# Kernel tuning notes

Measured on AMD Instinct MI355X. Metric: run time of the kernel, lower is better.

## Reference

```python
import jax, jax.numpy as jnp
import numpy as np

DECAY = 0.9      # LIF membrane decay per step
V_TH = 1.0       # spike threshold


def setup_inputs() -> dict:
    key = jax.random.key(0)
    k1, k2, k3, k4, k5 = jax.random.split(key, 5)
    B, D, N = 256, 1024, 2048
    density = 0.3
    external_inputs = jax.random.normal(k1, (B, D), dtype=jnp.float32)
    # nn.Linear(input_dim, num_neurons): weight [N, D], bias [N]
    W_in = jax.random.normal(k2, (N, D), dtype=jnp.float32) / np.sqrt(D)
    b_in = jnp.zeros((N,), dtype=jnp.float32)
    adj_weights = jax.random.normal(k3, (N, N), dtype=jnp.float32) * 0.01
    mask = (jax.random.uniform(k4, (N, N)) < density).astype(jnp.float32)
    mask = mask * (1.0 - jnp.eye(N, dtype=jnp.float32))  # zero diagonal
    return {
        "external_inputs": external_inputs,
        "W_in": W_in,
        "b_in": b_in,
        "adj_weights": adj_weights,
        "mask": mask,
        "time_steps": 64,
    }


def _spike(x):
    # Heaviside spike: 1 if membrane exceeds threshold
    return (x >= 0.0).astype(x.dtype)


def reference(external_inputs, W_in, b_in, adj_weights, mask, time_steps):
    B = external_inputs.shape[0]
    N = adj_weights.shape[0]
    I_ext = external_inputs @ W_in.T + b_in              # [B, N]
    W_eff = adj_weights * mask                           # [N, N]
    V0 = jnp.zeros((B, N), dtype=external_inputs.dtype)
    s0 = jnp.zeros((B, N), dtype=external_inputs.dtype)

    def step(carry, _):
        V, s = carry
        I_total = I_ext + s @ W_eff.T                    # recurrent current
        V = DECAY * V + I_total                          # LIF integration
        s_new = _spike(V - V_TH)
        V = V * (1.0 - s_new)                            # reset on spike
        return (V, s_new), s_new

    (_, _), spike_hist = jax.lax.scan(step, (V0, s0), None, length=time_steps)
    return spike_hist.mean(axis=0)                       # [B, N] firing rates
```

## Files before the change

kernel.cpp:

```cpp
#include <hip/hip_runtime.h>
#include <cstdint>
#include <cstddef>

#define N_NEU 2048
#define D_IN  1024
#define T_STEPS 64

typedef _Float16 f16x8 __attribute__((ext_vector_type(8)));
typedef _Float16 f16x4 __attribute__((ext_vector_type(4)));
typedef float    f32x4 __attribute__((ext_vector_type(4)));
typedef unsigned u32x4 __attribute__((ext_vector_type(4)));

#define MFMA16(a, b, c) __builtin_amdgcn_mfma_f32_16x16x32_f16((a), (b), (c), 0, 0, 0)


__device__ inline f16x8 expand8(unsigned b) {
  u32x4 t;
#pragma unroll
  for (int i = 0; i < 4; ++i) {
    unsigned m = (b >> (2 * i)) & 3u;
    unsigned s = (m | (m << 15)) & 0x00010001u;
    t[i] = s * 0x3C00u;
  }
  return __builtin_bit_cast(f16x8, t);
}

__global__ __launch_bounds__(256) void k_wsplit(const float* __restrict__ adj,
                                                const float* __restrict__ mask,
                                                _Float16* __restrict__ Wh,
                                                _Float16* __restrict__ Wl,
                                                unsigned long long* __restrict__ bmv) {
  const int idx = blockIdx.x * 256 + threadIdx.x;
  if (idx < 2 * 256 * 64) bmv[idx] = 0ull;
  const int total4 = (N_NEU * N_NEU) / 4;
  for (int i = idx; i < total4; i += gridDim.x * 256) {
    float4 a = ((const float4*)adj)[i];
    float4 m = ((const float4*)mask)[i];
    float w0 = a.x * m.x, w1 = a.y * m.y, w2 = a.z * m.z, w3 = a.w * m.w;
    f16x4 h, lo;
    h[0] = (_Float16)w0; lo[0] = (_Float16)((w0 - (float)h[0]) * 4096.0f);
    h[1] = (_Float16)w1; lo[1] = (_Float16)((w1 - (float)h[1]) * 4096.0f);
    h[2] = (_Float16)w2; lo[2] = (_Float16)((w2 - (float)h[2]) * 4096.0f);
    h[3] = (_Float16)w3; lo[3] = (_Float16)((w3 - (float)h[3]) * 4096.0f);
    ((f16x4*)Wh)[i] = h;
    ((f16x4*)Wl)[i] = lo;
  }
}

__global__ __launch_bounds__(256) void k_iext(const float* __restrict__ ext,
                                              const float* __restrict__ Win,
                                              const float* __restrict__ bin,
                                              float* __restrict__ Iext) {
  __shared__ float At[32][68];
  __shared__ float Bt[32][68];
  const int tid = threadIdx.x;
  const int b0 = (blockIdx.x & 3) * 64;
  const int n0 = (blockIdx.x >> 2) * 64;
  const int tx = tid & 15, ty = tid >> 4;
  float acc[4][4] = {};
  for (int kt = 0; kt < D_IN / 32; ++kt) {
    const int k0 = kt * 32;
#pragma unroll
    for (int i = 0; i < 8; ++i) {
      int e = tid + i * 256;
      int kk = e & 31, row = e >> 5;
      At[kk][row] = ext[(size_t)(b0 + row) * D_IN + k0 + kk];
      Bt[kk][row] = Win[(size_t)(n0 + row) * D_IN + k0 + kk];
    }
    __syncthreads();
    for (int kk = 0; kk < 32; ++kk) {
      f32x4 a = *(const f32x4*)&At[kk][ty * 4];
      f32x4 b = *(const f32x4*)&Bt[kk][tx * 4];
#pragma unroll
      for (int i = 0; i < 4; ++i)
#pragma unroll
        for (int j = 0; j < 4; ++j) acc[i][j] += a[i] * b[j];
    }
    __syncthreads();
  }
#pragma unroll
  for (int i = 0; i < 4; ++i)
#pragma unroll
    for (int j = 0; j < 4; ++j)
      Iext[(size_t)(b0 + ty * 4 + i) * N_NEU + n0 + tx * 4 + j] = acc[i][j] + bin[n0 + tx * 4 + j];
}

__global__ __launch_bounds__(512, 2) void k_fused11(
    const _Float16* __restrict__ Wh, const _Float16* __restrict__ Wl,
    const float* __restrict__ Iext, unsigned long long* __restrict__ bmv,
    float* __restrict__ out) {
  __shared__ float red[8 * 32 * 32];
  __shared__ unsigned bmA[32 * 64];
  __shared__ unsigned bmB[32 * 64];

  const int tid = threadIdx.x;
  const int lane = tid & 63;
  const int kw = tid >> 6;
  const int l15 = lane & 15;
  const int klo = lane >> 4;
  const int sh = klo * 8;
  const int gp = blockIdx.x >> 6;
  const int ns = blockIdx.x & 63;
  const int n0 = ns * 32;
  const int gA = gp, gB = gp + 4;
  const float inv4096 = 1.0f / 4096.0f;
  const f32x4 z4 = {0.f, 0.f, 0.f, 0.f};

  float IxA[2], IxB[2];
#pragma unroll
  for (int j = 0; j < 2; ++j) {
    IxA[j] = Iext[(size_t)(gA * 32 + j * 16 + (tid >> 5)) * N_NEU + n0 + (tid & 31)];
    IxB[j] = Iext[(size_t)(gB * 32 + j * 16 + (tid >> 5)) * N_NEU + n0 + (tid & 31)];
  }

  const _Float16* whb = Wh + (size_t)(n0 + l15) * N_NEU + kw * 256 + klo * 8;
  const _Float16* wlb = Wl + (size_t)(n0 + l15) * N_NEU + kw * 256 + klo * 8;
  f16x8 whf[2][8], wlf[2][8];
#pragma unroll
  for (int nt = 0; nt < 2; ++nt)
#pragma unroll
    for (int kcl = 0; kcl < 8; ++kcl) {
      whf[nt][kcl] = *(const f16x8*)(whb + nt * 16 * N_NEU + kcl * 32);
      wlf[nt][kcl] = *(const f16x8*)(wlb + nt * 16 * N_NEU + kcl * 32);
    }

  float VA[2] = {0.f, 0.f}, VB[2] = {0.f, 0.f};
  unsigned cA[2] = {0u, 0u}, cB[2] = {0u, 0u};
  unsigned long long vA[4], vB[4];

  auto spec_issue = [&](int g, int buf, unsigned long long (&v)[4]) {
    const unsigned long long* src = bmv + (size_t)buf * 16384 + (size_t)g * 2048 + tid;
#pragma unroll
    for (int i = 0; i < 4; ++i)
      v[i] = __hip_atomic_load(src + (size_t)i * 512, __ATOMIC_RELAXED, __HIP_MEMORY_SCOPE_AGENT);
  };
  auto check_retry = [&](int g, int buf, unsigned want, unsigned long long (&v)[4]) {
    const unsigned long long* src = bmv + (size_t)buf * 16384 + (size_t)g * 2048 + tid;
    unsigned need = 0u;
#pragma unroll
    for (int i = 0; i < 4; ++i)
      if ((unsigned)(v[i] >> 32) != want) need |= 1u << i;
    while (need) {
      __builtin_amdgcn_s_sleep(2);
#pragma unroll
      for (int i = 0; i < 4; ++i)
        if (need & (1u << i)) {
          v[i] = __hip_atomic_load(src + (size_t)i * 512,
                                   __ATOMIC_RELAXED, __HIP_MEMORY_SCOPE_AGENT);
          if ((unsigned)(v[i] >> 32) == want) need &= ~(1u << i);
        }
    }
  };
  auto stage = [&](unsigned* bm, const unsigned long long (&v)[4]) {
#pragma unroll
    for (int i = 0; i < 4; ++i) {
      const int w = i * 512 + tid, r = w >> 6, nsw = w & 63;
      bm[r * 64 + (nsw ^ ((r & 15) << 2))] = (unsigned)v[i];
    }
  };
  auto gemm = [&](const unsigned* bm, float (&cI)[2]) {
    f32x4 acch[2][2], accl[2][2];
#pragma unroll
    for (int mt = 0; mt < 2; ++mt)
#pragma unroll
      for (int nt = 0; nt < 2; ++nt) { acch[mt][nt] = z4; accl[mt][nt] = z4; }
#pragma unroll
    for (int mt = 0; mt < 2; ++mt) {
      const int row = mt * 16 + l15;
      const int swz = l15 << 2;
      const u32x4 q0 = *(const u32x4*)&bm[row * 64 + ((kw * 8) ^ swz)];
      const u32x4 q1 = *(const u32x4*)&bm[row * 64 + (((kw * 8) | 4) ^ swz)];
#pragma unroll
      for (int kcl = 0; kcl < 8; ++kcl) {
        const unsigned word = (kcl < 4) ? q0[kcl] : q1[kcl - 4];
        const f16x8 a = expand8((word >> sh) & 0xFFu);
        acch[mt][0] = MFMA16(a, whf[0][kcl], acch[mt][0]);
        accl[mt][0] = MFMA16(a, wlf[0][kcl], accl[mt][0]);
        acch[mt][1] = MFMA16(a, whf[1][kcl], acch[mt][1]);
        accl[mt][1] = MFMA16(a, wlf[1][kcl], accl[mt][1]);
      }
    }
    f32x4 cb[2][2];
#pragma unroll
    for (int mt = 0; mt < 2; ++mt)
#pragma unroll
      for (int nt = 0; nt < 2; ++nt) cb[mt][nt] = acch[mt][nt] + accl[mt][nt] * inv4096;
    const int cbn = lane & 15, rq = (lane >> 4) << 2;
#pragma unroll
    for (int mt = 0; mt < 2; ++mt)
#pragma unroll
      for (int nt = 0; nt < 2; ++nt) {
        const int col = nt * 16 + cbn;
        const int r0 = (mt * 16 + rq) ^ ((col & 7) << 2);
        *(f32x4*)(red + (kw * 32 + col) * 32 + r0) = cb[mt][nt];
      }
    __syncthreads();
#pragma unroll
    for (int j = 0; j < 2; ++j) {
      const int o = j * 512 + tid;
      const int row = o >> 5, col = o & 31;
      const int rs = row ^ ((col & 7) << 2);
      float s = 0.0f;
#pragma unroll
      for (int p = 0; p < 8; ++p) s += red[(p * 32 + col) * 32 + rs];
      cI[j] = s;
    }
  };
  auto lif = [&](const float (&cI)[2], const float (&Ix)[2], float (&V)[2],
                 unsigned (&cnt)[2], int g, int nbuf, unsigned tag, bool dostore) {
#pragma unroll
    for (int j = 0; j < 2; ++j) {
      float I = cI[j] + Ix[j];
      float v = 0.9f * V[j] + I;
      bool sp = (v - 1.0f) >= 0.0f;
      V[j] = sp ? 0.0f : v;
      cnt[j] += sp ? 1u : 0u;
      if (dostore) {
        unsigned long long ba = __ballot(sp);
        const int rowf = g * 32 + j * 16 + kw * 2;
        const unsigned long long tg = ((unsigned long long)tag) << 32;
        if (lane == 0)
          __hip_atomic_store(bmv + (size_t)nbuf * 16384 + (size_t)rowf * 64 + ns,
                             tg | (unsigned)ba, __ATOMIC_RELAXED, __HIP_MEMORY_SCOPE_AGENT);
        else if (lane == 32)
          __hip_atomic_store(bmv + (size_t)nbuf * 16384 + (size_t)(rowf + 1) * 64 + ns,
                             tg | (unsigned)(ba >> 32), __ATOMIC_RELAXED, __HIP_MEMORY_SCOPE_AGENT);
      }
    }
  };

  {
    const float cz[2] = {0.f, 0.f};
    lif(cz, IxA, VA, cA, gA, 1, 1u, true);
    lif(cz, IxB, VB, cB, gB, 1, 1u, true);
    spec_issue(gA, 1, vA);
  }

  for (int t = 1; t < T_STEPS; ++t) {
    const int cbuf = t & 1, nbuf = (t + 1) & 1;
    const bool last = (t == T_STEPS - 1);
    float cI[2];

    check_retry(gA, cbuf, (unsigned)t, vA);
    stage(bmA, vA);
    __syncthreads();
    spec_issue(gB, cbuf, vB);
    gemm(bmA, cI);
    lif(cI, IxA, VA, cA, gA, nbuf, (unsigned)(t + 1), !last);

    check_retry(gB, cbuf, (unsigned)t, vB);
    stage(bmB, vB);
    __syncthreads();
    if (!last) spec_issue(gA, nbuf, vA);
    gemm(bmB, cI);
    lif(cI, IxB, VB, cB, gB, nbuf, (unsigned)(t + 1), !last);
  }

#pragma unroll
  for (int j = 0; j < 2; ++j) {
    const int rA = gA * 32 + j * 16 + (tid >> 5);
    const int rB = gB * 32 + j * 16 + (tid >> 5);
    out[(size_t)rA * N_NEU + n0 + (tid & 31)] = (float)cA[j] * 0.015625f;
    out[(size_t)rB * N_NEU + n0 + (tid & 31)] = (float)cB[j] * 0.015625f;
  }
}

extern "C" void kernel_launch(void* const* d_in, const int* in_sizes, int n_in,
                              void* d_out, int out_size, void* d_ws, size_t ws_size,
                              hipStream_t stream) {
  (void)in_sizes; (void)n_in; (void)out_size; (void)ws_size;
  const float* ext  = (const float*)d_in[0];
  const float* Win  = (const float*)d_in[1];
  const float* bin  = (const float*)d_in[2];
  const float* adj  = (const float*)d_in[3];
  const float* mask = (const float*)d_in[4];
  unsigned char* ws = (unsigned char*)d_ws;

  _Float16* Wh   = (_Float16*)(ws);
  _Float16* Wl   = (_Float16*)(ws + (size_t)(8u << 20));
  float*    Iext = (float*)   (ws + (size_t)(16u << 20));
  unsigned long long* bmv = (unsigned long long*)(ws + (size_t)(18u << 20));
  float* out = (float*)d_out;

  hipLaunchKernelGGL(k_wsplit, dim3(2048), dim3(256), 0, stream, adj, mask, Wh, Wl, bmv);
  hipLaunchKernelGGL(k_iext,   dim3(128),  dim3(256), 0, stream, ext, Win, bin, Iext);
  hipLaunchKernelGGL(k_fused11, dim3(256), dim3(512), 0, stream,
                     Wh, Wl, Iext, bmv, out);
}
```

Measured before the change: 443.2 us.

## Split each block's batch work into four 16-row phases for finer pipelining

The persistent recurrent kernel now handles its 64 batch rows per time step as four 16-row phases instead of two 32-row groups. Spike bitmaps from other blocks are prefetched two phases ahead, and the reduction and staging buffers are smaller and padded rather than XOR-swizzled. The goal is to overlap the cross-block spike exchange wait with MFMA work and to shrink the per-phase latency on the step-to-step critical path. In exchange there are twice as many barriers and flag checks per step, and each phase does less MFMA work.

```diff
diff --git a/kernel.cpp b/kernel.cpp
--- a/kernel.cpp
+++ b/kernel.cpp
@@ -85,13 +85,12 @@
       Iext[(size_t)(b0 + ty * 4 + i) * N_NEU + n0 + tx * 4 + j] = acc[i][j] + bin[n0 + tx * 4 + j];
 }
 
-__global__ __launch_bounds__(512, 2) void k_fused11(
+__global__ __launch_bounds__(512, 2) void k_fused12(
     const _Float16* __restrict__ Wh, const _Float16* __restrict__ Wl,
     const float* __restrict__ Iext, unsigned long long* __restrict__ bmv,
     float* __restrict__ out) {
-  __shared__ float red[8 * 32 * 32];
-  __shared__ unsigned bmA[32 * 64];
-  __shared__ unsigned bmB[32 * 64];
+  __shared__ float red[8 * 32 * 20];
+  __shared__ unsigned bm[16 * 68];
 
   const int tid = threadIdx.x;
   const int lane = tid & 63;
@@ -102,16 +101,15 @@
   const int gp = blockIdx.x >> 6;
   const int ns = blockIdx.x & 63;
   const int n0 = ns * 32;
-  const int gA = gp, gB = gp + 4;
+  const int orow = tid >> 5;
+  const int ocol = tid & 31;
   const float inv4096 = 1.0f / 4096.0f;
   const f32x4 z4 = {0.f, 0.f, 0.f, 0.f};
 
-  float IxA[2], IxB[2];
-#pragma unroll
-  for (int j = 0; j < 2; ++j) {
-    IxA[j] = Iext[(size_t)(gA * 32 + j * 16 + (tid >> 5)) * N_NEU + n0 + (tid & 31)];
-    IxB[j] = Iext[(size_t)(gB * 32 + j * 16 + (tid >> 5)) * N_NEU + n0 + (tid & 31)];
-  }
+  const float Ix0 = Iext[(size_t)(gp * 64 +  0 + orow) * N_NEU + n0 + ocol];
+  const float Ix1 = Iext[(size_t)(gp * 64 + 16 + orow) * N_NEU + n0 + ocol];
+  const float Ix2 = Iext[(size_t)(gp * 64 + 32 + orow) * N_NEU + n0 + ocol];
+  const float Ix3 = Iext[(size_t)(gp * 64 + 48 + orow) * N_NEU + n0 + ocol];
 
   const _Float16* whb = Wh + (size_t)(n0 + l15) * N_NEU + kw * 256 + klo * 8;
   const _Float16* wlb = Wl + (size_t)(n0 + l15) * N_NEU + kw * 256 + klo * 8;
@@ -124,145 +122,114 @@
       wlf[nt][kcl] = *(const f16x8*)(wlb + nt * 16 * N_NEU + kcl * 32);
     }
 
-  float VA[2] = {0.f, 0.f}, VB[2] = {0.f, 0.f};
-  unsigned cA[2] = {0u, 0u}, cB[2] = {0u, 0u};
-  unsigned long long vA[4], vB[4];
-
-  auto spec_issue = [&](int g, int buf, unsigned long long (&v)[4]) {
-    const unsigned long long* src = bmv + (size_t)buf * 16384 + (size_t)g * 2048 + tid;
-#pragma unroll
-    for (int i = 0; i < 4; ++i)
-      v[i] = __hip_atomic_load(src + (size_t)i * 512, __ATOMIC_RELAXED, __HIP_MEMORY_SCOPE_AGENT);
-  };
-  auto check_retry = [&](int g, int buf, unsigned want, unsigned long long (&v)[4]) {
-    const unsigned long long* src = bmv + (size_t)buf * 16384 + (size_t)g * 2048 + tid;
+  float V0 = 0.f, V1 = 0.f, V2 = 0.f, V3 = 0.f;
+  unsigned c0 = 0u, c1 = 0u, c2 = 0u, c3 = 0u;
+  unsigned long long vqE[2], vqO[2];
+
+  auto issue = [&](int tI, int gI, unsigned long long (&v)[2]) {
+    const unsigned long long* src = bmv + (size_t)(tI & 1) * 16384
+        + (size_t)(gp * 64 + gI * 16) * 64 + tid;
+    v[0] = __hip_atomic_load(src, __ATOMIC_RELAXED, __HIP_MEMORY_SCOPE_AGENT);
+    v[1] = __hip_atomic_load(src + 512, __ATOMIC_RELAXED, __HIP_MEMORY_SCOPE_AGENT);
+  };
+  auto check = [&](int tC, int gC, unsigned long long (&v)[2]) {
+    const unsigned long long* src = bmv + (size_t)(tC & 1) * 16384
+        + (size_t)(gp * 64 + gC * 16) * 64 + tid;
+    const unsigned want = (unsigned)tC;
     unsigned need = 0u;
-#pragma unroll
-    for (int i = 0; i < 4; ++i)
-      if ((unsigned)(v[i] >> 32) != want) need |= 1u << i;
+    if ((unsigned)(v[0] >> 32) != want) need |= 1u;
+    if ((unsigned)(v[1] >> 32) != want) need |= 2u;
     while (need) {
-      __builtin_amdgcn_s_sleep(2);
-#pragma unroll
-      for (int i = 0; i < 4; ++i)
-        if (need & (1u << i)) {
-          v[i] = __hip_atomic_load(src + (size_t)i * 512,
-                                   __ATOMIC_RELAXED, __HIP_MEMORY_SCOPE_AGENT);
-          if ((unsigned)(v[i] >> 32) == want) need &= ~(1u << i);
-        }
-    }
-  };
-  auto stage = [&](unsigned* bm, const unsigned long long (&v)[4]) {
-#pragma unroll
-    for (int i = 0; i < 4; ++i) {
-      const int w = i * 512 + tid, r = w >> 6, nsw = w & 63;
-      bm[r * 64 + (nsw ^ ((r & 15) << 2))] = (unsigned)v[i];
-    }
-  };
-  auto gemm = [&](const unsigned* bm, float (&cI)[2]) {
-    f32x4 acch[2][2], accl[2][2];
-#pragma unroll
-    for (int mt = 0; mt < 2; ++mt)
-#pragma unroll
-      for (int nt = 0; nt < 2; ++nt) { acch[mt][nt] = z4; accl[mt][nt] = z4; }
-#pragma unroll
-    for (int mt = 0; mt < 2; ++mt) {
-      const int row = mt * 16 + l15;
-      const int swz = l15 << 2;
-      const u32x4 q0 = *(const u32x4*)&bm[row * 64 + ((kw * 8) ^ swz)];
-      const u32x4 q1 = *(const u32x4*)&bm[row * 64 + (((kw * 8) | 4) ^ swz)];
-#pragma unroll
-      for (int kcl = 0; kcl < 8; ++kcl) {
-        const unsigned word = (kcl < 4) ? q0[kcl] : q1[kcl - 4];
-        const f16x8 a = expand8((word >> sh) & 0xFFu);
-        acch[mt][0] = MFMA16(a, whf[0][kcl], acch[mt][0]);
-        accl[mt][0] = MFMA16(a, wlf[0][kcl], accl[mt][0]);
-        acch[mt][1] = MFMA16(a, whf[1][kcl], acch[mt][1]);
-        accl[mt][1] = MFMA16(a, wlf[1][kcl], accl[mt][1]);
+      __builtin_amdgcn_s_sleep(1);
+      if (need & 1u) {
+        v[0] = __hip_atomic_load(src, __ATOMIC_RELAXED, __HIP_MEMORY_SCOPE_AGENT);
+        if ((unsigned)(v[0] >> 32) == want) need &= ~1u;
       }
-    }
-    f32x4 cb[2][2];
-#pragma unroll
-    for (int mt = 0; mt < 2; ++mt)
-#pragma unroll
-      for (int nt = 0; nt < 2; ++nt) cb[mt][nt] = acch[mt][nt] + accl[mt][nt] * inv4096;
-    const int cbn = lane & 15, rq = (lane >> 4) << 2;
-#pragma unroll
-    for (int mt = 0; mt < 2; ++mt)
-#pragma unroll
-      for (int nt = 0; nt < 2; ++nt) {
-        const int col = nt * 16 + cbn;
-        const int r0 = (mt * 16 + rq) ^ ((col & 7) << 2);
-        *(f32x4*)(red + (kw * 32 + col) * 32 + r0) = cb[mt][nt];
+      if (need & 2u) {
+        v[1] = __hip_atomic_load(src + 512, __ATOMIC_RELAXED, __HIP_MEMORY_SCOPE_AGENT);
+        if ((unsigned)(v[1] >> 32) == want) need &= ~2u;
       }
-    __syncthreads();
-#pragma unroll
-    for (int j = 0; j < 2; ++j) {
-      const int o = j * 512 + tid;
-      const int row = o >> 5, col = o & 31;
-      const int rs = row ^ ((col & 7) << 2);
-      float s = 0.0f;
-#pragma unroll
-      for (int p = 0; p < 8; ++p) s += red[(p * 32 + col) * 32 + rs];
-      cI[j] = s;
-    }
-  };
-  auto lif = [&](const float (&cI)[2], const float (&Ix)[2], float (&V)[2],
-                 unsigned (&cnt)[2], int g, int nbuf, unsigned tag, bool dostore) {
-#pragma unroll
-    for (int j = 0; j < 2; ++j) {
-      float I = cI[j] + Ix[j];
-      float v = 0.9f * V[j] + I;
-      bool sp = (v - 1.0f) >= 0.0f;
-      V[j] = sp ? 0.0f : v;
-      cnt[j] += sp ? 1u : 0u;
-      if (dostore) {
-        unsigned long long ba = __ballot(sp);
-        const int rowf = g * 32 + j * 16 + kw * 2;
-        const unsigned long long tg = ((unsigned long long)tag) << 32;
-        if (lane == 0)
-          __hip_atomic_store(bmv + (size_t)nbuf * 16384 + (size_t)rowf * 64 + ns,
-                             tg | (unsigned)ba, __ATOMIC_RELAXED, __HIP_MEMORY_SCOPE_AGENT);
-        else if (lane == 32)
-          __hip_atomic_store(bmv + (size_t)nbuf * 16384 + (size_t)(rowf + 1) * 64 + ns,
-                             tg | (unsigned)(ba >> 32), __ATOMIC_RELAXED, __HIP_MEMORY_SCOPE_AGENT);
-      }
-    }
-  };
-
-  {
-    const float cz[2] = {0.f, 0.f};
-    lif(cz, IxA, VA, cA, gA, 1, 1u, true);
-    lif(cz, IxB, VB, cB, gB, 1, 1u, true);
-    spec_issue(gA, 1, vA);
-  }
+    }
+  };
+  auto stage = [&](const unsigned long long (&v)[2]) {
+    bm[(tid >> 6) * 68 + (tid & 63)] = (unsigned)v[0];
+    bm[((tid + 512) >> 6) * 68 + (tid & 63)] = (unsigned)v[1];
+  };
+  auto gemm_phase = [&](float& cI) {
+    f32x4 acch[2], accl[2];
+    acch[0] = z4; acch[1] = z4; accl[0] = z4; accl[1] = z4;
+    const u32x4 q0 = *(const u32x4*)&bm[l15 * 68 + kw * 8];
+    const u32x4 q1 = *(const u32x4*)&bm[l15 * 68 + kw * 8 + 4];
+#pragma unroll
+    for (int kcl = 0; kcl < 8; ++kcl) {
+      const unsigned word = (kcl < 4) ? q0[kcl] : q1[kcl - 4];
+      const f16x8 a = expand8((word >> sh) & 0xFFu);
+      acch[0] = MFMA16(a, whf[0][kcl], acch[0]);
+      accl[0] = MFMA16(a, wlf[0][kcl], accl[0]);
+      acch[1] = MFMA16(a, whf[1][kcl], acch[1]);
+      accl[1] = MFMA16(a, wlf[1][kcl], accl[1]);
+    }
+    const int rq = (lane >> 4) << 2;
+#pragma unroll
+    for (int nt = 0; nt < 2; ++nt) {
+      f32x4 cb = acch[nt] + accl[nt] * inv4096;
+      *(f32x4*)&red[(kw * 32 + nt * 16 + l15) * 20 + rq] = cb;
+    }
+    __syncthreads();
+    float s = 0.0f;
+#pragma unroll
+    for (int p = 0; p < 8; ++p) s += red[(p * 32 + ocol) * 20 + orow];
+    cI = s;
+  };
+  auto lifp = [&](float cI, float Ixg, float& Vg, unsigned& cg, int tL, int gL) {
+    float I = cI + Ixg;
+    float vm = 0.9f * Vg + I;
+    bool sp = (vm - 1.0f) >= 0.0f;
+    Vg = sp ? 0.0f : vm;
+    cg += sp ? 1u : 0u;
+    if (tL < T_STEPS - 1) {
+      unsigned long long ba = __ballot(sp);
+      const int rowf = gp * 64 + gL * 16 + kw * 2;
+      const unsigned long long tg = ((unsigned long long)(unsigned)(tL + 1)) << 32;
+      unsigned long long* dst = bmv + (size_t)((tL + 1) & 1) * 16384;
+      if (lane == 0)
+        __hip_atomic_store(dst + (size_t)rowf * 64 + ns, tg | (unsigned)ba,
+                           __ATOMIC_RELAXED, __HIP_MEMORY_SCOPE_AGENT);
+      else if (lane == 32)
+        __hip_atomic_store(dst + (size_t)(rowf + 1) * 64 + ns, tg | (unsigned)(ba >> 32),
+                           __ATOMIC_RELAXED, __HIP_MEMORY_SCOPE_AGENT);
+    }
+  };
+  auto phase = [&](int tP, int gP, float Ixg, float& Vg, unsigned& cg,
+                   unsigned long long (&v)[2], int tI, int gI, bool doIss) {
+    check(tP, gP, v);
+    stage(v);
+    __syncthreads();
+    if (doIss) issue(tI, gI, v);
+    float cI;
+    gemm_phase(cI);
+    lifp(cI, Ixg, Vg, cg, tP, gP);
+  };
+
+  lifp(0.0f, Ix0, V0, c0, 0, 0);
+  lifp(0.0f, Ix1, V1, c1, 0, 1);
+  lifp(0.0f, Ix2, V2, c2, 0, 2);
+  lifp(0.0f, Ix3, V3, c3, 0, 3);
+  issue(1, 0, vqE);
+  issue(1, 1, vqO);
 
   for (int t = 1; t < T_STEPS; ++t) {
-    const int cbuf = t & 1, nbuf = (t + 1) & 1;
-    const bool last = (t == T_STEPS - 1);
-    float cI[2];
-
-    check_retry(gA, cbuf, (unsigned)t, vA);
-    stage(bmA, vA);
-    __syncthreads();
-    spec_issue(gB, cbuf, vB);
-    gemm(bmA, cI);
-    lif(cI, IxA, VA, cA, gA, nbuf, (unsigned)(t + 1), !last);
-
-    check_retry(gB, cbuf, (unsigned)t, vB);
-    stage(bmB, vB);
-    __syncthreads();
-    if (!last) spec_issue(gA, nbuf, vA);
-    gemm(bmB, cI);
-    lif(cI, IxB, VB, cB, gB, nbuf, (unsigned)(t + 1), !last);
-  }
-
-#pragma unroll
-  for (int j = 0; j < 2; ++j) {
-    const int rA = gA * 32 + j * 16 + (tid >> 5);
-    const int rB = gB * 32 + j * 16 + (tid >> 5);
-    out[(size_t)rA * N_NEU + n0 + (tid & 31)] = (float)cA[j] * 0.015625f;
-    out[(size_t)rB * N_NEU + n0 + (tid & 31)] = (float)cB[j] * 0.015625f;
-  }
+    const bool nl = (t < T_STEPS - 1);
+    phase(t, 0, Ix0, V0, c0, vqE, t, 2, true);
+    phase(t, 1, Ix1, V1, c1, vqO, t, 3, true);
+    phase(t, 2, Ix2, V2, c2, vqE, t + 1, 0, nl);
+    phase(t, 3, Ix3, V3, c3, vqO, t + 1, 1, nl);
+  }
+
+  out[(size_t)(gp * 64 +  0 + orow) * N_NEU + n0 + ocol] = (float)c0 * 0.015625f;
+  out[(size_t)(gp * 64 + 16 + orow) * N_NEU + n0 + ocol] = (float)c1 * 0.015625f;
+  out[(size_t)(gp * 64 + 32 + orow) * N_NEU + n0 + ocol] = (float)c2 * 0.015625f;
+  out[(size_t)(gp * 64 + 48 + orow) * N_NEU + n0 + ocol] = (float)c3 * 0.015625f;
 }
 
 extern "C" void kernel_launch(void* const* d_in, const int* in_sizes, int n_in,
@@ -284,6 +251,6 @@
 
   hipLaunchKernelGGL(k_wsplit, dim3(2048), dim3(256), 0, stream, adj, mask, Wh, Wl, bmv);
   hipLaunchKernelGGL(k_iext,   dim3(128),  dim3(256), 0, stream, ext, Win, bin, Iext);
-  hipLaunchKernelGGL(k_fused11, dim3(256), dim3(512), 0, stream,
+  hipLaunchKernelGGL(k_fused12, dim3(256), dim3(512), 0, stream,
                      Wh, Wl, Iext, bmv, out);
 }
```

After: 441.1 us. About the same (-0.5%).
